# Kernel optimization log

Hardware: AMD Instinct MI355X
Metric: run time of the kernel (lower is better)

Reference implementation:

```python
import jax, jax.numpy as jnp
import numpy as np

N_NODES = 50000
N_EDGES = 800000
NFEAT, NHID, NCLASS = 512, 96, 40


def setup_inputs() -> dict:
    key = jax.random.key(0)
    ks = jax.random.split(key, 8)
    x = jax.random.normal(ks[0], (N_NODES, NFEAT), dtype=jnp.float32)
    edge_index = jax.random.randint(ks[1], (2, N_EDGES), 0, N_NODES, dtype=jnp.int64)
    edge_weight = jax.random.uniform(ks[2], (N_EDGES,), dtype=jnp.float32)
    # GCNConv weight/bias (glorot-ish scale) and Linear weight/bias
    W1 = jax.random.normal(ks[3], (NFEAT, NHID), dtype=jnp.float32) / np.sqrt(NFEAT)
    b1 = jnp.zeros((NHID,), dtype=jnp.float32)
    W2 = jax.random.normal(ks[4], (NHID, NCLASS), dtype=jnp.float32) / np.sqrt(NHID)
    b2 = jnp.zeros((NCLASS,), dtype=jnp.float32)
    return {"x": x, "edge_index": edge_index, "edge_weight": edge_weight,
            "W1": W1, "b1": b1, "W2": W2, "b2": b2}


def reference(x, edge_index, edge_weight, W1, b1, W2, b2):
    # GCNConv: dense transform then sparse aggregate (adj @ (x @ W1) + b1)
    support = x @ W1 + b1                       # [N, nhid]
    src, dst = edge_index[0], edge_index[1]
    msgs = support[src] * edge_weight[:, None]  # [E, nhid] gather + scale
    agg = jax.ops.segment_sum(msgs, dst, num_segments=N_NODES)  # [N, nhid]
    h = jax.nn.relu(agg)
    # dropout is identity in eval mode
    logits = h @ W2 + b2                        # [N, nclass]
    return jax.nn.log_softmax(logits, axis=1)
```

## Files before the change

### kernel.cpp

```cpp
#include <hip/hip_runtime.h>
#include <hip/hip_fp16.h>
#include <math.h>

static constexpr int N_NODES = 50000;
static constexpr int N_EDGES = 800000;
static constexpr int NFEAT = 512;
static constexpr int NHID = 96;
static constexpr int NCLASS = 40;
static constexpr int PREP_BLOCKS = 196;
static constexpr int GEMM1_BLOCKS = (N_NODES + 63) / 64;
static constexpr int BUCKET = 64;
static constexpr int W2LD = 104;
static constexpr int SC_GROUPS = 8;
static constexpr int SC_RANGE = N_NODES / SC_GROUPS;
static constexpr int SC_CHUNK = 2048;
static constexpr int SC_CHUNKS = (N_EDGES + SC_CHUNK - 1) / SC_CHUNK;
static constexpr int SCATTER_BLOCKS = SC_GROUPS * SC_CHUNKS;

typedef __bf16 bf16_t;
typedef __attribute__((ext_vector_type(8))) __bf16 bf16x8;
typedef __attribute__((ext_vector_type(4))) float f32x4;

__global__ __launch_bounds__(256) void k_zero(int* __restrict__ p, int n) {
    int i = blockIdx.x * 256 + threadIdx.x;
    if (i < n) p[i] = 0;
}

__global__ __launch_bounds__(256) void k_prep(const float* __restrict__ W1,
                                              const float* __restrict__ W2,
                                              bf16_t* __restrict__ w1t,
                                              bf16_t* __restrict__ w2t,
                                              int* __restrict__ cnt) {
    int e = blockIdx.x * 256 + threadIdx.x;
    if (e < N_NODES) cnt[e] = 0;
    if (e < NFEAT * NHID) {
        int k = e / NHID;
        int n = e - k * NHID;
        w1t[(size_t)n * NFEAT + k] = (bf16_t)W1[e];
    }
    if (e < 48 * NHID) {
        int n = e / NHID;
        int k = e - n * NHID;
        w2t[n * W2LD + k] = (n < NCLASS) ? (bf16_t)W2[k * NCLASS + n] : (bf16_t)0.f;
    }
}

static __device__ inline bf16x8 cvt8(float4 u, float4 v) {
    bf16x8 r;
    r[0] = (bf16_t)u.x; r[1] = (bf16_t)u.y; r[2] = (bf16_t)u.z; r[3] = (bf16_t)u.w;
    r[4] = (bf16_t)v.x; r[5] = (bf16_t)v.y; r[6] = (bf16_t)v.z; r[7] = (bf16_t)v.w;
    return r;
}

__global__ __launch_bounds__(256) void k_gemm1_scatter(
        const float* __restrict__ x, const bf16_t* __restrict__ w1t,
        const float* __restrict__ b1, bf16_t* __restrict__ support,
        const int* __restrict__ src, const int* __restrict__ dst,
        const float* __restrict__ ew, int* __restrict__ cnt,
        unsigned int* __restrict__ buck) {
    __shared__ bf16_t Bs[NHID * 64];
    const int tid = threadIdx.x;

    if (blockIdx.x >= GEMM1_BLOCKS) {
        const int si = blockIdx.x - GEMM1_BLOCKS;
        const int g = si & 7;
        const int c = si >> 3;
        const int lo = g * SC_RANGE;
        const int hi = lo + SC_RANGE;
        const int base = c * SC_CHUNK;
#pragma unroll
        for (int t = 0; t < SC_CHUNK / 256; ++t) {
            int i = base + t * 256 + tid;
            if (i < N_EDGES) {
                int d = dst[i];
                if (d >= lo && d < hi) {
                    int rank = atomicAdd(&cnt[d], 1);
                    if (rank < BUCKET) {
                        __half hh = __float2half(ew[i]);
                        unsigned short us = *reinterpret_cast<unsigned short*>(&hh);
                        buck[(size_t)d * BUCKET + rank] =
                            ((unsigned int)src[i] << 16) | (unsigned int)us;
                    }
                }
            }
        }
        return;
    }

    const int w = tid >> 6;
    const int l = tid & 63;
    const int row0 = blockIdx.x * 64;

    int arow = row0 + w * 16 + (l & 15);
    if (arow > N_NODES - 1) arow = N_NODES - 1;
    const float* ap = x + (size_t)arow * NFEAT + ((l >> 4) << 3);

    f32x4 acc[6];
#pragma unroll
    for (int nt = 0; nt < 6; ++nt) acc[nt] = (f32x4){0.f, 0.f, 0.f, 0.f};

    for (int kt = 0; kt < NFEAT; kt += 64) {
        float4 a0 = *reinterpret_cast<const float4*>(ap + kt);
        float4 a1 = *reinterpret_cast<const float4*>(ap + kt + 4);
        float4 a2 = *reinterpret_cast<const float4*>(ap + kt + 32);
        float4 a3 = *reinterpret_cast<const float4*>(ap + kt + 36);

        __syncthreads();
#pragma unroll
        for (int p = 0; p < 3; ++p) {
            int idx = tid + p * 256;
            int n = idx >> 3;
            int c4 = idx & 7;
            uint4 v = *reinterpret_cast<const uint4*>(w1t + (size_t)n * NFEAT + kt + c4 * 8);
            int ba = (n * 128 + c4 * 16) ^ ((n & 7) << 4);
            *reinterpret_cast<uint4*>(reinterpret_cast<char*>(Bs) + ba) = v;
        }
        __syncthreads();

        bf16x8 af0 = cvt8(a0, a1);
        bf16x8 af1 = cvt8(a2, a3);
        const int koff = (l >> 4) << 4;
#pragma unroll
        for (int nt = 0; nt < 6; ++nt) {
            int n = nt * 16 + (l & 15);
            int ba0 = (n * 128 + koff) ^ ((n & 7) << 4);
            int ba1 = (n * 128 + 64 + koff) ^ ((n & 7) << 4);
            bf16x8 bf0 = *reinterpret_cast<const bf16x8*>(reinterpret_cast<const char*>(Bs) + ba0);
            bf16x8 bf1 = *reinterpret_cast<const bf16x8*>(reinterpret_cast<const char*>(Bs) + ba1);
            acc[nt] = __builtin_amdgcn_mfma_f32_16x16x32_bf16(af0, bf0, acc[nt], 0, 0, 0);
            acc[nt] = __builtin_amdgcn_mfma_f32_16x16x32_bf16(af1, bf1, acc[nt], 0, 0, 0);
        }
    }

    const int col16 = l & 15;
    const int rq = l >> 4;
#pragma unroll
    for (int nt = 0; nt < 6; ++nt) {
        int col = nt * 16 + col16;
        float bv = b1[col];
#pragma unroll
        for (int r = 0; r < 4; ++r) {
            int row = row0 + w * 16 + rq * 4 + r;
            if (row < N_NODES)
                support[(size_t)row * NHID + col] = (bf16_t)(acc[nt][r] + bv);
        }
    }
}

static __device__ inline float dec_w(unsigned int v) {
    unsigned short us = (unsigned short)(v & 0xffffu);
    __half hh = *reinterpret_cast<__half*>(&us);
    return __half2float(hh);
}

__global__ __launch_bounds__(256) void k_agg(const bf16_t* __restrict__ support,
                                             const int* __restrict__ cnt,
                                             const unsigned int* __restrict__ buck,
                                             bf16_t* __restrict__ h) {
    const int g = blockIdx.x * 8 + (threadIdx.x >> 5);
    const int l = threadIdx.x & 31;
    if (g >= N_NODES) return;
    int deg = cnt[g];
    if (deg > BUCKET) deg = BUCKET;
    const unsigned int* bk = buck + (size_t)g * BUCKET;
    float a0 = 0.f, a1 = 0.f, a2 = 0.f;
    int e = 0;
    for (; e + 4 <= deg; e += 4) {
        uint4 q = *reinterpret_cast<const uint4*>(bk + e);
        const bf16_t* r0 = support + (size_t)(q.x >> 16) * NHID;
        const bf16_t* r1 = support + (size_t)(q.y >> 16) * NHID;
        const bf16_t* r2 = support + (size_t)(q.z >> 16) * NHID;
        const bf16_t* r3 = support + (size_t)(q.w >> 16) * NHID;
        float w0 = dec_w(q.x), w1 = dec_w(q.y), w2 = dec_w(q.z), w3 = dec_w(q.w);
        float v00 = (float)r0[l], v01 = (float)r0[l + 32], v02 = (float)r0[l + 64];
        float v10 = (float)r1[l], v11 = (float)r1[l + 32], v12 = (float)r1[l + 64];
        float v20 = (float)r2[l], v21 = (float)r2[l + 32], v22 = (float)r2[l + 64];
        float v30 = (float)r3[l], v31 = (float)r3[l + 32], v32 = (float)r3[l + 64];
        a0 = fmaf(w0, v00, a0); a1 = fmaf(w0, v01, a1); a2 = fmaf(w0, v02, a2);
        a0 = fmaf(w1, v10, a0); a1 = fmaf(w1, v11, a1); a2 = fmaf(w1, v12, a2);
        a0 = fmaf(w2, v20, a0); a1 = fmaf(w2, v21, a1); a2 = fmaf(w2, v22, a2);
        a0 = fmaf(w3, v30, a0); a1 = fmaf(w3, v31, a1); a2 = fmaf(w3, v32, a2);
    }
    for (; e < deg; ++e) {
        unsigned int v = bk[e];
        const bf16_t* r = support + (size_t)(v >> 16) * NHID;
        float wv = dec_w(v);
        a0 = fmaf(wv, (float)r[l], a0);
        a1 = fmaf(wv, (float)r[l + 32], a1);
        a2 = fmaf(wv, (float)r[l + 64], a2);
    }
    bf16_t* hr = h + (size_t)g * NHID;
    hr[l]      = (bf16_t)fmaxf(a0, 0.f);
    hr[l + 32] = (bf16_t)fmaxf(a1, 0.f);
    hr[l + 64] = (bf16_t)fmaxf(a2, 0.f);
}

__global__ __launch_bounds__(256) void k_gemm2_mfma(const bf16_t* __restrict__ h,
                                                    const bf16_t* __restrict__ w2t,
                                                    const float* __restrict__ b2,
                                                    float* __restrict__ out) {
    __shared__ bf16_t Bs[48 * W2LD];
    const int tid = threadIdx.x;
#pragma unroll
    for (int i = tid; i < 48 * W2LD / 8; i += 256)
        *reinterpret_cast<uint4*>(Bs + i * 8) =
            *reinterpret_cast<const uint4*>(w2t + i * 8);

    const int w = tid >> 6;
    const int l = tid & 63;
    const int row0 = blockIdx.x * 64 + w * 16;
    int arow = row0 + (l & 15);
    if (arow > N_NODES - 1) arow = N_NODES - 1;
    const bf16_t* ap = h + (size_t)arow * NHID + ((l >> 4) << 3);

    f32x4 acc[3];
#pragma unroll
    for (int nt = 0; nt < 3; ++nt) acc[nt] = (f32x4){0.f, 0.f, 0.f, 0.f};
    __syncthreads();

#pragma unroll
    for (int ks = 0; ks < 3; ++ks) {
        bf16x8 af = *reinterpret_cast<const bf16x8*>(ap + ks * 32);
#pragma unroll
        for (int nt = 0; nt < 3; ++nt) {
            int n = nt * 16 + (l & 15);
            bf16x8 bf = *reinterpret_cast<const bf16x8*>(
                &Bs[n * W2LD + ks * 32 + ((l >> 4) << 3)]);
            acc[nt] = __builtin_amdgcn_mfma_f32_16x16x32_bf16(af, bf, acc[nt], 0, 0, 0);
        }
    }

    const int c16 = l & 15;
    float bv[3];
    bool val[3];
#pragma unroll
    for (int nt = 0; nt < 3; ++nt) {
        int col = nt * 16 + c16;
        val[nt] = col < NCLASS;
        bv[nt] = val[nt] ? b2[col] : 0.f;
    }
#pragma unroll
    for (int r = 0; r < 4; ++r) {
        float lg[3];
        float m = -1e30f;
#pragma unroll
        for (int nt = 0; nt < 3; ++nt) {
            lg[nt] = acc[nt][r] + bv[nt];
            if (val[nt]) m = fmaxf(m, lg[nt]);
        }
#pragma unroll
        for (int off = 1; off < 16; off <<= 1) m = fmaxf(m, __shfl_xor(m, off));
        float s = 0.f;
#pragma unroll
        for (int nt = 0; nt < 3; ++nt)
            if (val[nt]) s += __expf(lg[nt] - m);
#pragma unroll
        for (int off = 1; off < 16; off <<= 1) s += __shfl_xor(s, off);
        float lse = __logf(s);
        int row = row0 + ((l >> 4) << 2) + r;
        if (row < N_NODES) {
#pragma unroll
            for (int nt = 0; nt < 3; ++nt)
                if (val[nt])
                    out[(size_t)row * NCLASS + nt * 16 + c16] = lg[nt] - m - lse;
        }
    }
}

__global__ __launch_bounds__(256) void k_agg_atomic(const bf16_t* __restrict__ support,
                                                    const int* __restrict__ src,
                                                    const int* __restrict__ dst,
                                                    const float* __restrict__ ew,
                                                    float* __restrict__ hf) {
    int e = blockIdx.x * 8 + (threadIdx.x >> 5);
    int l = threadIdx.x & 31;
    if (e >= N_EDGES) return;
    int s = src[e];
    int d = dst[e];
    float w = ew[e];
    const bf16_t* r = support + (size_t)s * NHID;
    float* hd = hf + (size_t)d * NHID;
    atomicAdd(&hd[l], w * (float)r[l]);
    atomicAdd(&hd[l + 32], w * (float)r[l + 32]);
    atomicAdd(&hd[l + 64], w * (float)r[l + 64]);
}

__global__ __launch_bounds__(256) void k_gemm2_fb(const float* __restrict__ hf,
                                                  const bf16_t* __restrict__ w2t,
                                                  const float* __restrict__ b2,
                                                  float* __restrict__ out) {
    __shared__ bf16_t hs[64][W2LD];
    __shared__ bf16_t Bs[48 * W2LD];
    const int tid = threadIdx.x;
#pragma unroll
    for (int i = tid; i < 48 * W2LD / 8; i += 256)
        *reinterpret_cast<uint4*>(Bs + i * 8) =
            *reinterpret_cast<const uint4*>(w2t + i * 8);
    const int row0 = blockIdx.x * 64;
    for (int i = tid; i < 64 * NHID; i += 256) {
        int r = i / NHID, c = i - r * NHID;
        int row = row0 + r;
        float v = (row < N_NODES) ? fmaxf(hf[(size_t)row * NHID + c], 0.f) : 0.f;
        hs[r][c] = (bf16_t)v;
    }
    __syncthreads();
    const int w = tid >> 6;
    const int l64 = tid & 63;
    const int r16 = l64 & 15;
    const int kq = l64 >> 4;
    f32x4 acc[3];
#pragma unroll
    for (int nt = 0; nt < 3; ++nt) acc[nt] = (f32x4){0.f, 0.f, 0.f, 0.f};
#pragma unroll
    for (int ks = 0; ks < 3; ++ks) {
        bf16x8 af = *reinterpret_cast<const bf16x8*>(&hs[w * 16 + r16][ks * 32 + (kq << 3)]);
#pragma unroll
        for (int nt = 0; nt < 3; ++nt) {
            int n = nt * 16 + r16;
            bf16x8 bf = *reinterpret_cast<const bf16x8*>(&Bs[n * W2LD + ks * 32 + (kq << 3)]);
            acc[nt] = __builtin_amdgcn_mfma_f32_16x16x32_bf16(af, bf, acc[nt], 0, 0, 0);
        }
    }
    float bv[3];
    bool val[3];
#pragma unroll
    for (int nt = 0; nt < 3; ++nt) {
        int col = nt * 16 + r16;
        val[nt] = col < NCLASS;
        bv[nt] = val[nt] ? b2[col] : 0.f;
    }
#pragma unroll
    for (int r = 0; r < 4; ++r) {
        float lg[3];
        float m = -1e30f;
#pragma unroll
        for (int nt = 0; nt < 3; ++nt) {
            lg[nt] = acc[nt][r] + bv[nt];
            if (val[nt]) m = fmaxf(m, lg[nt]);
        }
#pragma unroll
        for (int off = 1; off < 16; off <<= 1) m = fmaxf(m, __shfl_xor(m, off));
        float s = 0.f;
#pragma unroll
        for (int nt = 0; nt < 3; ++nt)
            if (val[nt]) s += __expf(lg[nt] - m);
#pragma unroll
        for (int off = 1; off < 16; off <<= 1) s += __shfl_xor(s, off);
        float lse = __logf(s);
        int row = row0 + w * 16 + kq * 4 + r;
        if (row < N_NODES) {
#pragma unroll
            for (int nt = 0; nt < 3; ++nt)
                if (val[nt])
                    out[(size_t)row * NCLASS + nt * 16 + r16] = lg[nt] - m - lse;
        }
    }
}

extern "C" void kernel_launch(void* const* d_in, const int* in_sizes, int n_in,
                              void* d_out, int out_size, void* d_ws, size_t ws_size,
                              hipStream_t stream) {
    const float* x  = (const float*)d_in[0];
    const int* ei   = (const int*)d_in[1];
    const float* ew = (const float*)d_in[2];
    const float* W1 = (const float*)d_in[3];
    const float* b1 = (const float*)d_in[4];
    const float* W2 = (const float*)d_in[5];
    const float* b2 = (const float*)d_in[6];
    float* out = (float*)d_out;
    const int* src = ei;
    const int* dst = ei + N_EDGES;

    char* ws = (char*)d_ws;
    size_t off = 0;
    auto alloc = [&](size_t bytes) -> void* {
        void* p = ws + off;
        off = (off + bytes + 255) & ~(size_t)255;
        return p;
    };
    bf16_t* support = (bf16_t*)alloc((size_t)N_NODES * NHID * 2);
    bf16_t* h       = (bf16_t*)alloc((size_t)N_NODES * NHID * 2);
    bf16_t* w1t     = (bf16_t*)alloc((size_t)NHID * NFEAT * 2);
    bf16_t* w2t     = (bf16_t*)alloc((size_t)48 * W2LD * 2);
    int* cnt        = (int*)alloc((size_t)N_NODES * 4);
    unsigned int* buck = (unsigned int*)alloc((size_t)N_NODES * BUCKET * 4);
    const bool fits = (off <= ws_size);
    float* hf       = (float*)alloc((size_t)N_NODES * NHID * 4);

    k_prep<<<PREP_BLOCKS, 256, 0, stream>>>(W1, W2, w1t, w2t, cnt);

    if (fits) {
        k_gemm1_scatter<<<GEMM1_BLOCKS + SCATTER_BLOCKS, 256, 0, stream>>>(
            x, w1t, b1, support, src, dst, ew, cnt, buck);
        k_agg<<<(N_NODES + 7) / 8, 256, 0, stream>>>(support, cnt, buck, h);
        k_gemm2_mfma<<<GEMM1_BLOCKS, 256, 0, stream>>>(h, w2t, b2, out);
    } else {
        k_gemm1_scatter<<<GEMM1_BLOCKS, 256, 0, stream>>>(
            x, w1t, b1, support, src, dst, ew, cnt, buck);
        k_zero<<<(N_NODES * NHID + 255) / 256, 256, 0, stream>>>((int*)hf, N_NODES * NHID);
        k_agg_atomic<<<(N_EDGES + 7) / 8, 256, 0, stream>>>(support, src, dst, ew, hf);
        k_gemm2_fb<<<GEMM1_BLOCKS, 256, 0, stream>>>(hf, w2t, b2, out);
    }
}
```

Before: 103.1 us.

## Double-buffer x loads in registers and widen GEMM1 K-tile to 128

GEMM1 now stages W1 in 128-wide K chunks in LDS (doubling shared memory) and prefetches the next chunk of x rows into registers while the MFMAs on the current chunk run. This halves the number of barrier pairs and overlaps global x loads with compute, so the memory-bound x stream should be hidden better. The cost is more registers (16 float4 live) and LDS, which may reduce occupancy.

```diff
diff --git a/kernel.cpp b/kernel.cpp
--- a/kernel.cpp
+++ b/kernel.cpp
@@ -58,7 +58,7 @@
         const int* __restrict__ src, const int* __restrict__ dst,
         const float* __restrict__ ew, int* __restrict__ cnt,
         unsigned int* __restrict__ buck) {
-    __shared__ bf16_t Bs[NHID * 64];
+    __shared__ bf16_t Bs[NHID * 128];
     const int tid = threadIdx.x;
 
     if (blockIdx.x >= GEMM1_BLOCKS) {
@@ -99,36 +99,51 @@
 #pragma unroll
     for (int nt = 0; nt < 6; ++nt) acc[nt] = (f32x4){0.f, 0.f, 0.f, 0.f};
 
-    for (int kt = 0; kt < NFEAT; kt += 64) {
-        float4 a0 = *reinterpret_cast<const float4*>(ap + kt);
-        float4 a1 = *reinterpret_cast<const float4*>(ap + kt + 4);
-        float4 a2 = *reinterpret_cast<const float4*>(ap + kt + 32);
-        float4 a3 = *reinterpret_cast<const float4*>(ap + kt + 36);
-
+    const int koff = (l >> 4) << 4;
+
+    float4 xa[8];
+#pragma unroll
+    for (int i = 0; i < 8; ++i)
+        xa[i] = *reinterpret_cast<const float4*>(ap + (i >> 1) * 32 + (i & 1) * 4);
+
+#pragma unroll
+    for (int kc = 0; kc < 4; ++kc) {
+        const int kt = kc * 128;
         __syncthreads();
 #pragma unroll
-        for (int p = 0; p < 3; ++p) {
+        for (int p = 0; p < 6; ++p) {
             int idx = tid + p * 256;
-            int n = idx >> 3;
-            int c4 = idx & 7;
+            int n = idx >> 4;
+            int c4 = idx & 15;
             uint4 v = *reinterpret_cast<const uint4*>(w1t + (size_t)n * NFEAT + kt + c4 * 8);
-            int ba = (n * 128 + c4 * 16) ^ ((n & 7) << 4);
+            int ba = (n * 256 + c4 * 16) ^ ((n & 7) << 4);
             *reinterpret_cast<uint4*>(reinterpret_cast<char*>(Bs) + ba) = v;
         }
         __syncthreads();
 
-        bf16x8 af0 = cvt8(a0, a1);
-        bf16x8 af1 = cvt8(a2, a3);
-        const int koff = (l >> 4) << 4;
-#pragma unroll
-        for (int nt = 0; nt < 6; ++nt) {
-            int n = nt * 16 + (l & 15);
-            int ba0 = (n * 128 + koff) ^ ((n & 7) << 4);
-            int ba1 = (n * 128 + 64 + koff) ^ ((n & 7) << 4);
-            bf16x8 bf0 = *reinterpret_cast<const bf16x8*>(reinterpret_cast<const char*>(Bs) + ba0);
-            bf16x8 bf1 = *reinterpret_cast<const bf16x8*>(reinterpret_cast<const char*>(Bs) + ba1);
-            acc[nt] = __builtin_amdgcn_mfma_f32_16x16x32_bf16(af0, bf0, acc[nt], 0, 0, 0);
-            acc[nt] = __builtin_amdgcn_mfma_f32_16x16x32_bf16(af1, bf1, acc[nt], 0, 0, 0);
+        float4 xb[8];
+        if (kc < 3) {
+#pragma unroll
+            for (int i = 0; i < 8; ++i)
+                xb[i] = *reinterpret_cast<const float4*>(
+                    ap + kt + 128 + (i >> 1) * 32 + (i & 1) * 4);
+        }
+
+#pragma unroll
+        for (int ks = 0; ks < 4; ++ks) {
+            bf16x8 af = cvt8(xa[2 * ks], xa[2 * ks + 1]);
+#pragma unroll
+            for (int nt = 0; nt < 6; ++nt) {
+                int n = nt * 16 + (l & 15);
+                int ba = (n * 256 + ks * 64 + koff) ^ ((n & 7) << 4);
+                bf16x8 bf = *reinterpret_cast<const bf16x8*>(
+                    reinterpret_cast<const char*>(Bs) + ba);
+                acc[nt] = __builtin_amdgcn_mfma_f32_16x16x32_bf16(af, bf, acc[nt], 0, 0, 0);
+            }
+        }
+        if (kc < 3) {
+#pragma unroll
+            for (int i = 0; i < 8; ++i) xa[i] = xb[i];
         }
     }
 
```

Result: slower. 114.8 us (+11.3%).
